# Kernel tuning notes

Hardware: AMD Instinct MI355X
Metric: run time of the kernel (lower is better)

## Reference

```python
import jax, jax.numpy as jnp
import numpy as np

N_NODES = 100000
N_EDGES = 1600000
N_FEAT = 64
DIM = 32
N_CLASSES = 10
N_GRAPHS = 64
BN_EPS = 1e-5


def setup_inputs() -> dict:
    key = jax.random.key(0)
    ks = jax.random.split(key, 20)
    x = jax.random.normal(ks[0], (N_NODES, N_FEAT), dtype=jnp.float32)
    edge_index = jax.random.randint(ks[1], (2, N_EDGES), 0, N_NODES, dtype=jnp.int64)
    batch = jnp.sort(jax.random.randint(ks[2], (N_NODES,), 0, N_GRAPHS, dtype=jnp.int64))
    s = 0.1
    # conv1 MLP (in=N_FEAT)
    w1a = jax.random.normal(ks[3], (N_FEAT, DIM), dtype=jnp.float32) * s
    b1a = jnp.zeros((DIM,), jnp.float32)
    w1b = jax.random.normal(ks[4], (DIM, DIM), dtype=jnp.float32) * s
    b1b = jnp.zeros((DIM,), jnp.float32)
    # convs 2-5 MLPs stacked [4, DIM, DIM]
    Wa = jax.random.normal(ks[5], (4, DIM, DIM), dtype=jnp.float32) * s
    Ba = jnp.zeros((4, DIM), jnp.float32)
    Wb = jax.random.normal(ks[6], (4, DIM, DIM), dtype=jnp.float32) * s
    Bb = jnp.zeros((4, DIM), jnp.float32)
    bn_gamma = jnp.ones((5, DIM), jnp.float32)
    bn_beta = jnp.zeros((5, DIM), jnp.float32)
    fc1_w = jax.random.normal(ks[7], (DIM, DIM), dtype=jnp.float32) * s
    fc1_b = jnp.zeros((DIM,), jnp.float32)
    fc2_w = jax.random.normal(ks[8], (DIM, N_CLASSES), dtype=jnp.float32) * s
    fc2_b = jnp.zeros((N_CLASSES,), jnp.float32)
    return dict(x=x, edge_index=edge_index, batch=batch,
                w1a=w1a, b1a=b1a, w1b=w1b, b1b=b1b,
                Wa=Wa, Ba=Ba, Wb=Wb, Bb=Bb,
                bn_gamma=bn_gamma, bn_beta=bn_beta,
                fc1_w=fc1_w, fc1_b=fc1_b, fc2_w=fc2_w, fc2_b=fc2_b)


def _gin_aggr(x, src, dst):
    # sum_{j in N(i)} x_j  + x_i   (eps = 0)
    agg = jax.ops.segment_sum(x[src], dst, num_segments=N_NODES)
    return x + agg


def _mlp(h, wa, ba, wb, bb):
    return jax.nn.relu(h @ wa + ba) @ wb + bb


def _bn(h, gamma, beta):
    mu = jnp.mean(h, axis=0)
    var = jnp.mean((h - mu) ** 2, axis=0)  # biased, torch BN training mode
    return (h - mu) * jax.lax.rsqrt(var + BN_EPS) * gamma + beta


def reference(x, edge_index, batch, w1a, b1a, w1b, b1b, Wa, Ba, Wb, Bb,
              bn_gamma, bn_beta, fc1_w, fc1_b, fc2_w, fc2_b):
    src, dst = edge_index[0], edge_index[1]
    # layer 1 (num_features -> dim)
    h = _mlp(_gin_aggr(x, src, dst), w1a, b1a, w1b, b1b)
    h = _bn(jax.nn.relu(h), bn_gamma[0], bn_beta[0])
    # layers 2-5 (dim -> dim)
    for i in range(4):
        h = _mlp(_gin_aggr(h, src, dst), Wa[i], Ba[i], Wb[i], Bb[i])
        h = _bn(jax.nn.relu(h), bn_gamma[i + 1], bn_beta[i + 1])
    # global add pool over graphs
    g = jax.ops.segment_sum(h, batch, num_segments=N_GRAPHS)  # [G, dim]
    g = jax.nn.relu(g @ fc1_w + fc1_b)
    # dropout: eval mode -> identity
    return g @ fc2_w + fc2_b  # [G, num_classes]
```

## Files before the change

kernel.cpp:

```cpp
#include <hip/hip_runtime.h>

#define NN 100000
#define NE 1600000
#define NF 64
#define DM 32
#define NG 64
#define NC 10
#define BN_EPS 1e-5f

#define BSHIFT 8
#define NBUCK ((NN + 255) >> 8)
#define CHUNK 8192
#define NCH ((NE + CHUNK - 1) / CHUNK)

__global__ __launch_bounds__(256) void binA_k(const int* __restrict__ ei,
                                              int* __restrict__ bcnt) {
    __shared__ int h[NBUCK];
    for (int i = threadIdx.x; i < NBUCK; i += 256) h[i] = 0;
    __syncthreads();
    long long base = (long long)blockIdx.x * CHUNK;
    int n = (int)((NE - base < CHUNK) ? (NE - base) : CHUNK);
    for (int i = threadIdx.x; i < n; i += 256) {
        int d = ei[NE + base + i];
        atomicAdd(&h[d >> BSHIFT], 1);
    }
    __syncthreads();
    for (int i = threadIdx.x; i < NBUCK; i += 256)
        if (h[i]) atomicAdd(&bcnt[i], h[i]);
}

__global__ __launch_bounds__(512) void binB_k(const int* __restrict__ bcnt,
                                              int* __restrict__ bbase,
                                              int* __restrict__ bcur) {
    __shared__ int s[512];
    int t = threadIdx.x;
    int v = (t < NBUCK) ? bcnt[t] : 0;
    s[t] = v;
    __syncthreads();
    int acc = v;
    for (int off = 1; off < 512; off <<= 1) {
        int add = (t >= off) ? s[t - off] : 0;
        __syncthreads();
        acc += add;
        s[t] = acc;
        __syncthreads();
    }
    if (t < NBUCK) { bbase[t] = acc - v; bcur[t] = acc - v; }
    if (t == 0) bbase[NBUCK] = NE;
}

__global__ __launch_bounds__(256) void binC_k(const int* __restrict__ ei,
                                              int* __restrict__ bcur,
                                              int2* __restrict__ binned) {
    __shared__ int cnt[NBUCK];
    __shared__ int ofs[NBUCK];
    __shared__ int idx[NBUCK];
    for (int i = threadIdx.x; i < NBUCK; i += 256) { cnt[i] = 0; idx[i] = 0; }
    __syncthreads();
    long long base = (long long)blockIdx.x * CHUNK;
    int n = (int)((NE - base < CHUNK) ? (NE - base) : CHUNK);
    int d[CHUNK / 256];
#pragma unroll
    for (int k = 0; k < CHUNK / 256; k++) {
        int i = threadIdx.x + k * 256;
        int dd = (i < n) ? ei[NE + base + i] : -1;
        d[k] = dd;
        if (dd >= 0) atomicAdd(&cnt[dd >> BSHIFT], 1);
    }
    __syncthreads();
    for (int i = threadIdx.x; i < NBUCK; i += 256)
        if (cnt[i]) ofs[i] = atomicAdd(&bcur[i], cnt[i]);
    __syncthreads();
#pragma unroll
    for (int k = 0; k < CHUNK / 256; k++) {
        int i = threadIdx.x + k * 256;
        if (i < n) {
            int src = ei[base + i];
            int b = d[k] >> BSHIFT;
            int l = atomicAdd(&idx[b], 1);
            binned[ofs[b] + l] = make_int2(src, d[k]);
        }
    }
}

__global__ __launch_bounds__(256) void binD_k(const int2* __restrict__ binned,
                                              const int* __restrict__ bbase,
                                              int* __restrict__ rowptr,
                                              int* __restrict__ csr) {
    __shared__ int cnt[256];
    __shared__ int cur[256];
    __shared__ int s[256];
    int b = blockIdx.x;
    int n0 = b << BSHIFT;
    int e0 = bbase[b], e1 = bbase[b + 1];
    int t = threadIdx.x;
    cnt[t] = 0;
    __syncthreads();
    for (int e = e0 + t; e < e1; e += 256) atomicAdd(&cnt[binned[e].y - n0], 1);
    __syncthreads();
    int v = cnt[t];
    s[t] = v;
    __syncthreads();
    int acc = v;
    for (int off = 1; off < 256; off <<= 1) {
        int add = (t >= off) ? s[t - off] : 0;
        __syncthreads();
        acc += add;
        s[t] = acc;
        __syncthreads();
    }
    int base = e0 + acc - v;
    int node = n0 + t;
    if (node < NN) rowptr[node] = base;
    cur[t] = base;
    if (b == NBUCK - 1 && t == 0) rowptr[NN] = NE;
    __syncthreads();
    for (int e = e0 + t; e < e1; e += 256) {
        int2 ed = binned[e];
        int p = atomicAdd(&cur[ed.y - n0], 1);
        csr[p] = ed.x;
    }
}

__global__ __launch_bounds__(256) void gather64_k(const float* __restrict__ x,
                                                  const int* __restrict__ rowptr,
                                                  const int* __restrict__ csr,
                                                  float* __restrict__ agg) {
    int tid = threadIdx.x;
    int node = blockIdx.x * 16 + tid / 16;
    int l = tid % 16;
    if (node >= NN) return;
    int s = rowptr[node], e = rowptr[node + 1];
    const float4* x4 = reinterpret_cast<const float4*>(x);
    float4 acc = make_float4(0.f, 0.f, 0.f, 0.f);
    for (int i = s; i < e; i++) {
        int src = csr[i];
        float4 v = x4[(long long)src * 16 + l];
        acc.x += v.x; acc.y += v.y; acc.z += v.z; acc.w += v.w;
    }
    reinterpret_cast<float4*>(agg)[(long long)node * 16 + l] = acc;
}

__global__ __launch_bounds__(256) void gather_bn_k(const float* __restrict__ h,
                                                   const int* __restrict__ rowptr,
                                                   const int* __restrict__ csr,
                                                   float* __restrict__ agg,
                                                   const float* __restrict__ st,
                                                   const float* __restrict__ gamma,
                                                   const float* __restrict__ beta) {
    int tid = threadIdx.x;
    int node = blockIdx.x * 32 + tid / 8;
    int l = tid % 8;
    if (node >= NN) return;
    const float invn = 1.0f / NN;
    float sc[4], sh[4];
#pragma unroll
    for (int c = 0; c < 4; c++) {
        int f = 4 * l + c;
        float mu = st[f] * invn;
        float var = st[32 + f] * invn - mu * mu;
        float scale = rsqrtf(var + BN_EPS) * gamma[f];
        sc[c] = scale;
        sh[c] = beta[f] - mu * scale;
    }
    int s = rowptr[node], e = rowptr[node + 1];
    const float4* h4 = reinterpret_cast<const float4*>(h);
    float4 acc = make_float4(0.f, 0.f, 0.f, 0.f);
    for (int i = s; i < e; i++) {
        int src = csr[i];
        float4 v = h4[(long long)src * 8 + l];
        acc.x += v.x; acc.y += v.y; acc.z += v.z; acc.w += v.w;
    }
    float deg = (float)(e - s);
    acc.x = acc.x * sc[0] + deg * sh[0];
    acc.y = acc.y * sc[1] + deg * sh[1];
    acc.z = acc.z * sc[2] + deg * sh[2];
    acc.w = acc.w * sc[3] + deg * sh[3];
    reinterpret_cast<float4*>(agg)[(long long)node * 8 + l] = acc;
}

__global__ __launch_bounds__(256) void mlp1_k(const float* __restrict__ x,
                                              const float* __restrict__ agg,
                                              const float* __restrict__ wa,
                                              const float* __restrict__ ba,
                                              const float* __restrict__ wb,
                                              const float* __restrict__ bb,
                                              float* __restrict__ out,
                                              float* __restrict__ stats) {
    __shared__ float sWa[64 * 32];
    __shared__ float sWb[32 * 32];
    __shared__ float sBa[32], sBb[32];
    __shared__ float sSum[4 * 32], sSq[4 * 32];
    int tid = threadIdx.x;
    for (int i = tid; i < 64 * 32; i += 256) sWa[i] = wa[i];
    for (int i = tid; i < 32 * 32; i += 256) sWb[i] = wb[i];
    if (tid < 32) { sBa[tid] = ba[tid]; sBb[tid] = bb[tid]; }
    __syncthreads();

    int node = blockIdx.x * 256 + tid;
    float r[32];
    if (node < NN) {
        float t[32];
#pragma unroll
        for (int j = 0; j < 32; j++) t[j] = sBa[j];
        const float4* xr = reinterpret_cast<const float4*>(x + (long long)node * 64);
        const float4* ar = reinterpret_cast<const float4*>(agg + (long long)node * 64);
        const float4* w4 = reinterpret_cast<const float4*>(sWa);
        for (int k4 = 0; k4 < 16; k4++) {
            float4 xv = xr[k4];
            float4 av = ar[k4];
            float a0 = xv.x + av.x, a1 = xv.y + av.y, a2 = xv.z + av.z, a3 = xv.w + av.w;
            int kb = k4 * 4;
#pragma unroll
            for (int q = 0; q < 8; q++) {
                float4 w0 = w4[(kb + 0) * 8 + q];
                float4 w1 = w4[(kb + 1) * 8 + q];
                float4 w2 = w4[(kb + 2) * 8 + q];
                float4 w3 = w4[(kb + 3) * 8 + q];
                t[4 * q + 0] += a0 * w0.x + a1 * w1.x + a2 * w2.x + a3 * w3.x;
                t[4 * q + 1] += a0 * w0.y + a1 * w1.y + a2 * w2.y + a3 * w3.y;
                t[4 * q + 2] += a0 * w0.z + a1 * w1.z + a2 * w2.z + a3 * w3.z;
                t[4 * q + 3] += a0 * w0.w + a1 * w1.w + a2 * w2.w + a3 * w3.w;
            }
        }
#pragma unroll
        for (int j = 0; j < 32; j++) t[j] = fmaxf(t[j], 0.f);
#pragma unroll
        for (int j = 0; j < 32; j++) r[j] = sBb[j];
        const float4* v4 = reinterpret_cast<const float4*>(sWb);
        for (int k = 0; k < 32; k++) {
            float a = t[k];
#pragma unroll
            for (int q = 0; q < 8; q++) {
                float4 w = v4[k * 8 + q];
                r[4 * q + 0] += a * w.x;
                r[4 * q + 1] += a * w.y;
                r[4 * q + 2] += a * w.z;
                r[4 * q + 3] += a * w.w;
            }
        }
#pragma unroll
        for (int j = 0; j < 32; j++) r[j] = fmaxf(r[j], 0.f);
        float4* orow = reinterpret_cast<float4*>(out + (long long)node * 32);
#pragma unroll
        for (int q = 0; q < 8; q++) {
            float4 o;
            o.x = r[4 * q]; o.y = r[4 * q + 1]; o.z = r[4 * q + 2]; o.w = r[4 * q + 3];
            orow[q] = o;
        }
    } else {
#pragma unroll
        for (int j = 0; j < 32; j++) r[j] = 0.f;
    }

    int lane = tid & 63, wid = tid >> 6;
#pragma unroll
    for (int j = 0; j < 32; j++) {
        float v = r[j], v2 = v * v;
#pragma unroll
        for (int off = 32; off >= 1; off >>= 1) {
            v += __shfl_down(v, off, 64);
            v2 += __shfl_down(v2, off, 64);
        }
        if (lane == 0) { sSum[wid * 32 + j] = v; sSq[wid * 32 + j] = v2; }
    }
    __syncthreads();
    if (tid < 32) {
        float a = sSum[tid] + sSum[32 + tid] + sSum[64 + tid] + sSum[96 + tid];
        float b = sSq[tid] + sSq[32 + tid] + sSq[64 + tid] + sSq[96 + tid];
        atomicAdd(&stats[tid], a);
        atomicAdd(&stats[32 + tid], b);
    }
}

__global__ __launch_bounds__(256) void mlp32_bn_k(float* __restrict__ h,
                                                  const float* __restrict__ agg,
                                                  const float* __restrict__ wa,
                                                  const float* __restrict__ ba,
                                                  const float* __restrict__ wb,
                                                  const float* __restrict__ bb,
                                                  const float* __restrict__ st,
                                                  const float* __restrict__ gamma,
                                                  const float* __restrict__ beta,
                                                  float* __restrict__ statsOut) {
    __shared__ float sWa[32 * 32];
    __shared__ float sWb[32 * 32];
    __shared__ float sBa[32], sBb[32];
    __shared__ float sSc[32], sSh[32];
    __shared__ float sSum[4 * 32], sSq[4 * 32];
    int tid = threadIdx.x;
    for (int i = tid; i < 32 * 32; i += 256) { sWa[i] = wa[i]; sWb[i] = wb[i]; }
    if (tid < 32) {
        sBa[tid] = ba[tid]; sBb[tid] = bb[tid];
        const float invn = 1.0f / NN;
        float mu = st[tid] * invn;
        float var = st[32 + tid] * invn - mu * mu;
        float scale = rsqrtf(var + BN_EPS) * gamma[tid];
        sSc[tid] = scale;
        sSh[tid] = beta[tid] - mu * scale;
    }
    __syncthreads();

    int node = blockIdx.x * 256 + tid;
    float r[32];
    if (node < NN) {
        float t[32];
#pragma unroll
        for (int j = 0; j < 32; j++) t[j] = sBa[j];
        const float4* hr = reinterpret_cast<const float4*>(h + (long long)node * 32);
        const float4* ar = reinterpret_cast<const float4*>(agg + (long long)node * 32);
        const float4* w4 = reinterpret_cast<const float4*>(sWa);
        for (int k4 = 0; k4 < 8; k4++) {
            float4 xv = hr[k4];
            float4 av = ar[k4];
            int kb = k4 * 4;
            float a0 = xv.x * sSc[kb + 0] + sSh[kb + 0] + av.x;
            float a1 = xv.y * sSc[kb + 1] + sSh[kb + 1] + av.y;
            float a2 = xv.z * sSc[kb + 2] + sSh[kb + 2] + av.z;
            float a3 = xv.w * sSc[kb + 3] + sSh[kb + 3] + av.w;
#pragma unroll
            for (int q = 0; q < 8; q++) {
                float4 w0 = w4[(kb + 0) * 8 + q];
                float4 w1 = w4[(kb + 1) * 8 + q];
                float4 w2 = w4[(kb + 2) * 8 + q];
                float4 w3 = w4[(kb + 3) * 8 + q];
                t[4 * q + 0] += a0 * w0.x + a1 * w1.x + a2 * w2.x + a3 * w3.x;
                t[4 * q + 1] += a0 * w0.y + a1 * w1.y + a2 * w2.y + a3 * w3.y;
                t[4 * q + 2] += a0 * w0.z + a1 * w1.z + a2 * w2.z + a3 * w3.z;
                t[4 * q + 3] += a0 * w0.w + a1 * w1.w + a2 * w2.w + a3 * w3.w;
            }
        }
#pragma unroll
        for (int j = 0; j < 32; j++) t[j] = fmaxf(t[j], 0.f);
#pragma unroll
        for (int j = 0; j < 32; j++) r[j] = sBb[j];
        const float4* v4 = reinterpret_cast<const float4*>(sWb);
        for (int k = 0; k < 32; k++) {
            float a = t[k];
#pragma unroll
            for (int q = 0; q < 8; q++) {
                float4 w = v4[k * 8 + q];
                r[4 * q + 0] += a * w.x;
                r[4 * q + 1] += a * w.y;
                r[4 * q + 2] += a * w.z;
                r[4 * q + 3] += a * w.w;
            }
        }
#pragma unroll
        for (int j = 0; j < 32; j++) r[j] = fmaxf(r[j], 0.f);
        float4* orow = reinterpret_cast<float4*>(h + (long long)node * 32);
#pragma unroll
        for (int q = 0; q < 8; q++) {
            float4 o;
            o.x = r[4 * q]; o.y = r[4 * q + 1]; o.z = r[4 * q + 2]; o.w = r[4 * q + 3];
            orow[q] = o;
        }
    } else {
#pragma unroll
        for (int j = 0; j < 32; j++) r[j] = 0.f;
    }

    int lane = tid & 63, wid = tid >> 6;
#pragma unroll
    for (int j = 0; j < 32; j++) {
        float v = r[j], v2 = v * v;
#pragma unroll
        for (int off = 32; off >= 1; off >>= 1) {
            v += __shfl_down(v, off, 64);
            v2 += __shfl_down(v2, off, 64);
        }
        if (lane == 0) { sSum[wid * 32 + j] = v; sSq[wid * 32 + j] = v2; }
    }
    __syncthreads();
    if (tid < 32) {
        float a = sSum[tid] + sSum[32 + tid] + sSum[64 + tid] + sSum[96 + tid];
        float b = sSq[tid] + sSq[32 + tid] + sSq[64 + tid] + sSq[96 + tid];
        atomicAdd(&statsOut[tid], a);
        atomicAdd(&statsOut[32 + tid], b);
    }
}

#define POOL_NPB 512
__global__ __launch_bounds__(256) void pool_bn_k(const float* __restrict__ h,
                                                 const int* __restrict__ batch,
                                                 const float* __restrict__ st,
                                                 const float* __restrict__ gamma,
                                                 const float* __restrict__ beta,
                                                 float* __restrict__ pooled) {
    int tid = threadIdx.x;
    int f = tid & 31;
    int p = tid >> 5;
    int n0 = blockIdx.x * POOL_NPB + p * (POOL_NPB / 8);
    int n1 = n0 + POOL_NPB / 8;
    if (n1 > NN) n1 = NN;
    if (n0 >= NN) return;
    const float invn = 1.0f / NN;
    float mu = st[f] * invn;
    float var = st[32 + f] * invn - mu * mu;
    float sc = rsqrtf(var + BN_EPS) * gamma[f];
    float sh = beta[f] - mu * sc;
    float acc = 0.f;
    int cur = batch[n0];
    for (int n = n0; n < n1; n++) {
        int g = batch[n];
        if (g != cur) {
            atomicAdd(&pooled[cur * 32 + f], acc);
            cur = g;
            acc = 0.f;
        }
        acc += h[(long long)n * 32 + f] * sc + sh;
    }
    atomicAdd(&pooled[cur * 32 + f], acc);
}

__global__ __launch_bounds__(64) void final_k(const float* __restrict__ pooled,
                                              const float* __restrict__ w1,
                                              const float* __restrict__ b1,
                                              const float* __restrict__ w2,
                                              const float* __restrict__ b2,
                                              float* __restrict__ out) {
    int g = threadIdx.x;
    if (g >= NG) return;
    float t[32];
#pragma unroll
    for (int j = 0; j < 32; j++) t[j] = b1[j];
    for (int k = 0; k < 32; k++) {
        float a = pooled[g * 32 + k];
#pragma unroll
        for (int j = 0; j < 32; j++) t[j] += a * w1[k * 32 + j];
    }
#pragma unroll
    for (int j = 0; j < 32; j++) t[j] = fmaxf(t[j], 0.f);
    for (int c = 0; c < NC; c++) {
        float o = b2[c];
#pragma unroll
        for (int k = 0; k < 32; k++) o += t[k] * w2[k * NC + c];
        out[g * NC + c] = o;
    }
}

extern "C" void kernel_launch(void* const* d_in, const int* in_sizes, int n_in,
                              void* d_out, int out_size, void* d_ws, size_t ws_size,
                              hipStream_t stream) {
    const float* x = (const float*)d_in[0];
    const int* ei = (const int*)d_in[1];
    const int* batch = (const int*)d_in[2];
    const float* w1a = (const float*)d_in[3];
    const float* b1a = (const float*)d_in[4];
    const float* w1b = (const float*)d_in[5];
    const float* b1b = (const float*)d_in[6];
    const float* Wa = (const float*)d_in[7];
    const float* Ba = (const float*)d_in[8];
    const float* Wb = (const float*)d_in[9];
    const float* Bb = (const float*)d_in[10];
    const float* bn_gamma = (const float*)d_in[11];
    const float* bn_beta = (const float*)d_in[12];
    const float* fc1w = (const float*)d_in[13];
    const float* fc1b = (const float*)d_in[14];
    const float* fc2w = (const float*)d_in[15];
    const float* fc2b = (const float*)d_in[16];
    float* out = (float*)d_out;

    float* ws = (float*)d_ws;
    float* agg = ws;
    float* hb = agg + (size_t)NN * 64;
    float* stats_all = hb + (size_t)NN * 32;
    float* pooled = stats_all + 5 * 64;
    int2* binned = (int2*)(pooled + NG * 32);
    int* bcnt = (int*)(binned + NE);
    int* bbase = bcnt + NBUCK;
    int* bcur = bbase + NBUCK + 1;
    int* rowptr = bcur + NBUCK;
    int* csr = rowptr + NN + 1;

    const int nodeBlocks = (NN + 255) / 256;

    hipMemsetAsync(bcnt, 0, NBUCK * sizeof(int), stream);
    binA_k<<<NCH, 256, 0, stream>>>(ei, bcnt);
    binB_k<<<1, 512, 0, stream>>>(bcnt, bbase, bcur);
    binC_k<<<NCH, 256, 0, stream>>>(ei, bcur, binned);
    binD_k<<<NBUCK, 256, 0, stream>>>(binned, bbase, rowptr, csr);

    hipMemsetAsync(stats_all, 0, 5 * 64 * sizeof(float), stream);
    hipMemsetAsync(pooled, 0, NG * 32 * sizeof(float), stream);

    gather64_k<<<NN / 16, 256, 0, stream>>>(x, rowptr, csr, agg);
    mlp1_k<<<nodeBlocks, 256, 0, stream>>>(x, agg, w1a, b1a, w1b, b1b, hb, stats_all);

    for (int i = 0; i < 4; i++) {
        const float* st = stats_all + i * 64;
        const float* g = bn_gamma + i * 32;
        const float* be = bn_beta + i * 32;
        gather_bn_k<<<NN / 32, 256, 0, stream>>>(hb, rowptr, csr, agg, st, g, be);
        mlp32_bn_k<<<nodeBlocks, 256, 0, stream>>>(hb, agg, Wa + i * 1024, Ba + i * 32,
                                                   Wb + i * 1024, Bb + i * 32,
                                                   st, g, be, stats_all + (i + 1) * 64);
    }

    pool_bn_k<<<(NN + POOL_NPB - 1) / POOL_NPB, 256, 0, stream>>>(
        hb, batch, stats_all + 4 * 64, bn_gamma + 4 * 32, bn_beta + 4 * 32, pooled);
    final_k<<<1, 64, 0, stream>>>(pooled, fc1w, fc1b, fc2w, fc2b, out);
}
```

Baseline: 589.4 us.

## Project layer-1 features before aggregation, pack binned edges, unroll gathers

Layer 1 now multiplies x by W1a before the neighbour aggregation (linearity), so the gather reads 32-float rows instead of 64-float rows. This halves the random-access traffic of the first gather, at the cost of an extra projection kernel and an intermediate buffer. Binned edges are packed into one 32-bit word (src<<8 | local dst), which halves binning traffic but limits src to 24 bits. Gather loops are unrolled by two with separate accumulators to keep more loads in flight, and the two memsets are merged into one.

```diff
diff --git a/kernel.cpp b/kernel.cpp
--- a/kernel.cpp
+++ b/kernel.cpp
@@ -51,7 +51,7 @@
 
 __global__ __launch_bounds__(256) void binC_k(const int* __restrict__ ei,
                                               int* __restrict__ bcur,
-                                              int2* __restrict__ binned) {
+                                              unsigned* __restrict__ binned) {
     __shared__ int cnt[NBUCK];
     __shared__ int ofs[NBUCK];
     __shared__ int idx[NBUCK];
@@ -75,15 +75,15 @@
     for (int k = 0; k < CHUNK / 256; k++) {
         int i = threadIdx.x + k * 256;
         if (i < n) {
-            int src = ei[base + i];
+            unsigned src = (unsigned)ei[base + i];
             int b = d[k] >> BSHIFT;
             int l = atomicAdd(&idx[b], 1);
-            binned[ofs[b] + l] = make_int2(src, d[k]);
-        }
-    }
-}
-
-__global__ __launch_bounds__(256) void binD_k(const int2* __restrict__ binned,
+            binned[ofs[b] + l] = (src << 8) | (unsigned)(d[k] & 255);
+        }
+    }
+}
+
+__global__ __launch_bounds__(256) void binD_k(const unsigned* __restrict__ binned,
                                               const int* __restrict__ bbase,
                                               int* __restrict__ rowptr,
                                               int* __restrict__ csr) {
@@ -91,12 +91,11 @@
     __shared__ int cur[256];
     __shared__ int s[256];
     int b = blockIdx.x;
-    int n0 = b << BSHIFT;
     int e0 = bbase[b], e1 = bbase[b + 1];
     int t = threadIdx.x;
     cnt[t] = 0;
     __syncthreads();
-    for (int e = e0 + t; e < e1; e += 256) atomicAdd(&cnt[binned[e].y - n0], 1);
+    for (int e = e0 + t; e < e1; e += 256) atomicAdd(&cnt[binned[e] & 255u], 1);
     __syncthreads();
     int v = cnt[t];
     s[t] = v;
@@ -110,35 +109,82 @@
         __syncthreads();
     }
     int base = e0 + acc - v;
-    int node = n0 + t;
+    int node = (b << BSHIFT) + t;
     if (node < NN) rowptr[node] = base;
     cur[t] = base;
     if (b == NBUCK - 1 && t == 0) rowptr[NN] = NE;
     __syncthreads();
     for (int e = e0 + t; e < e1; e += 256) {
-        int2 ed = binned[e];
-        int p = atomicAdd(&cur[ed.y - n0], 1);
-        csr[p] = ed.x;
-    }
-}
-
-__global__ __launch_bounds__(256) void gather64_k(const float* __restrict__ x,
+        unsigned w = binned[e];
+        int p = atomicAdd(&cur[w & 255u], 1);
+        csr[p] = (int)(w >> 8);
+    }
+}
+
+__global__ __launch_bounds__(256) void pre1_k(const float* __restrict__ x,
+                                              const float* __restrict__ wa,
+                                              float* __restrict__ y) {
+    __shared__ float sWa[64 * 32];
+    int tid = threadIdx.x;
+    for (int i = tid; i < 64 * 32; i += 256) sWa[i] = wa[i];
+    __syncthreads();
+    int node = blockIdx.x * 256 + tid;
+    if (node >= NN) return;
+    float t[32];
+#pragma unroll
+    for (int j = 0; j < 32; j++) t[j] = 0.f;
+    const float4* xr = reinterpret_cast<const float4*>(x + (long long)node * 64);
+    const float4* w4 = reinterpret_cast<const float4*>(sWa);
+    for (int k4 = 0; k4 < 16; k4++) {
+        float4 xv = xr[k4];
+        int kb = k4 * 4;
+#pragma unroll
+        for (int q = 0; q < 8; q++) {
+            float4 w0 = w4[(kb + 0) * 8 + q];
+            float4 w1 = w4[(kb + 1) * 8 + q];
+            float4 w2 = w4[(kb + 2) * 8 + q];
+            float4 w3 = w4[(kb + 3) * 8 + q];
+            t[4 * q + 0] += xv.x * w0.x + xv.y * w1.x + xv.z * w2.x + xv.w * w3.x;
+            t[4 * q + 1] += xv.x * w0.y + xv.y * w1.y + xv.z * w2.y + xv.w * w3.y;
+            t[4 * q + 2] += xv.x * w0.z + xv.y * w1.z + xv.z * w2.z + xv.w * w3.z;
+            t[4 * q + 3] += xv.x * w0.w + xv.y * w1.w + xv.z * w2.w + xv.w * w3.w;
+        }
+    }
+    float4* yr = reinterpret_cast<float4*>(y + (long long)node * 32);
+#pragma unroll
+    for (int q = 0; q < 8; q++) {
+        float4 o;
+        o.x = t[4 * q]; o.y = t[4 * q + 1]; o.z = t[4 * q + 2]; o.w = t[4 * q + 3];
+        yr[q] = o;
+    }
+}
+
+__global__ __launch_bounds__(256) void gather32_k(const float* __restrict__ y,
                                                   const int* __restrict__ rowptr,
                                                   const int* __restrict__ csr,
                                                   float* __restrict__ agg) {
     int tid = threadIdx.x;
-    int node = blockIdx.x * 16 + tid / 16;
-    int l = tid % 16;
+    int node = blockIdx.x * 32 + tid / 8;
+    int l = tid % 8;
     if (node >= NN) return;
     int s = rowptr[node], e = rowptr[node + 1];
-    const float4* x4 = reinterpret_cast<const float4*>(x);
-    float4 acc = make_float4(0.f, 0.f, 0.f, 0.f);
-    for (int i = s; i < e; i++) {
-        int src = csr[i];
-        float4 v = x4[(long long)src * 16 + l];
-        acc.x += v.x; acc.y += v.y; acc.z += v.z; acc.w += v.w;
-    }
-    reinterpret_cast<float4*>(agg)[(long long)node * 16 + l] = acc;
+    const float4* y4 = reinterpret_cast<const float4*>(y);
+    float4 a0 = make_float4(0.f, 0.f, 0.f, 0.f);
+    float4 a1 = make_float4(0.f, 0.f, 0.f, 0.f);
+    int i = s;
+    for (; i + 2 <= e; i += 2) {
+        int s0 = csr[i], s1 = csr[i + 1];
+        float4 v0 = y4[(long long)s0 * 8 + l];
+        float4 v1 = y4[(long long)s1 * 8 + l];
+        a0.x += v0.x; a0.y += v0.y; a0.z += v0.z; a0.w += v0.w;
+        a1.x += v1.x; a1.y += v1.y; a1.z += v1.z; a1.w += v1.w;
+    }
+    if (i < e) {
+        float4 v = y4[(long long)csr[i] * 8 + l];
+        a0.x += v.x; a0.y += v.y; a0.z += v.z; a0.w += v.w;
+    }
+    a0.x += a1.x; a0.y += a1.y; a0.z += a1.z; a0.w += a1.w;
+    reinterpret_cast<float4*>(agg)[(long long)node * 8 + l] = a0;
 }
 
 __global__ __launch_bounds__(256) void gather_bn_k(const float* __restrict__ h,
@@ -165,34 +211,40 @@
     }
     int s = rowptr[node], e = rowptr[node + 1];
     const float4* h4 = reinterpret_cast<const float4*>(h);
-    float4 acc = make_float4(0.f, 0.f, 0.f, 0.f);
-    for (int i = s; i < e; i++) {
-        int src = csr[i];
-        float4 v = h4[(long long)src * 8 + l];
-        acc.x += v.x; acc.y += v.y; acc.z += v.z; acc.w += v.w;
-    }
+    float4 a0 = make_float4(0.f, 0.f, 0.f, 0.f);
+    float4 a1 = make_float4(0.f, 0.f, 0.f, 0.f);
+    int i = s;
+    for (; i + 2 <= e; i += 2) {
+        int s0 = csr[i], s1 = csr[i + 1];
+        float4 v0 = h4[(long long)s0 * 8 + l];
+        float4 v1 = h4[(long long)s1 * 8 + l];
+        a0.x += v0.x; a0.y += v0.y; a0.z += v0.z; a0.w += v0.w;
+        a1.x += v1.x; a1.y += v1.y; a1.z += v1.z; a1.w += v1.w;
+    }
+    if (i < e) {
+        float4 v = h4[(long long)csr[i] * 8 + l];
+        a0.x += v.x; a0.y += v.y; a0.z += v.z; a0.w += v.w;
+    }
+    a0.x += a1.x; a0.y += a1.y; a0.z += a1.z; a0.w += a1.w;
     float deg = (float)(e - s);
-    acc.x = acc.x * sc[0] + deg * sh[0];
-    acc.y = acc.y * sc[1] + deg * sh[1];
-    acc.z = acc.z * sc[2] + deg * sh[2];
-    acc.w = acc.w * sc[3] + deg * sh[3];
-    reinterpret_cast<float4*>(agg)[(long long)node * 8 + l] = acc;
-}
-
-__global__ __launch_bounds__(256) void mlp1_k(const float* __restrict__ x,
-                                              const float* __restrict__ agg,
-                                              const float* __restrict__ wa,
-                                              const float* __restrict__ ba,
-                                              const float* __restrict__ wb,
-                                              const float* __restrict__ bb,
-                                              float* __restrict__ out,
-                                              float* __restrict__ stats) {
-    __shared__ float sWa[64 * 32];
+    a0.x = a0.x * sc[0] + deg * sh[0];
+    a0.y = a0.y * sc[1] + deg * sh[1];
+    a0.z = a0.z * sc[2] + deg * sh[2];
+    a0.w = a0.w * sc[3] + deg * sh[3];
+    reinterpret_cast<float4*>(agg)[(long long)node * 8 + l] = a0;
+}
+
+__global__ __launch_bounds__(256) void mlp1b_k(const float* __restrict__ y,
+                                               const float* __restrict__ agg,
+                                               const float* __restrict__ ba,
+                                               const float* __restrict__ wb,
+                                               const float* __restrict__ bb,
+                                               float* __restrict__ out,
+                                               float* __restrict__ stats) {
     __shared__ float sWb[32 * 32];
     __shared__ float sBa[32], sBb[32];
     __shared__ float sSum[4 * 32], sSq[4 * 32];
     int tid = threadIdx.x;
-    for (int i = tid; i < 64 * 32; i += 256) sWa[i] = wa[i];
     for (int i = tid; i < 32 * 32; i += 256) sWb[i] = wb[i];
     if (tid < 32) { sBa[tid] = ba[tid]; sBb[tid] = bb[tid]; }
     __syncthreads();
@@ -200,43 +252,29 @@
     int node = blockIdx.x * 256 + tid;
     float r[32];
     if (node < NN) {
-        float t[32];
-#pragma unroll
-        for (int j = 0; j < 32; j++) t[j] = sBa[j];
-        const float4* xr = reinterpret_cast<const float4*>(x + (long long)node * 64);
-        const float4* ar = reinterpret_cast<const float4*>(agg + (long long)node * 64);
-        const float4* w4 = reinterpret_cast<const float4*>(sWa);
-        for (int k4 = 0; k4 < 16; k4++) {
-            float4 xv = xr[k4];
-            float4 av = ar[k4];
-            float a0 = xv.x + av.x, a1 = xv.y + av.y, a2 = xv.z + av.z, a3 = xv.w + av.w;
-            int kb = k4 * 4;
-#pragma unroll
-            for (int q = 0; q < 8; q++) {
-                float4 w0 = w4[(kb + 0) * 8 + q];
-                float4 w1 = w4[(kb + 1) * 8 + q];
-                float4 w2 = w4[(kb + 2) * 8 + q];
-                float4 w3 = w4[(kb + 3) * 8 + q];
-                t[4 * q + 0] += a0 * w0.x + a1 * w1.x + a2 * w2.x + a3 * w3.x;
-                t[4 * q + 1] += a0 * w0.y + a1 * w1.y + a2 * w2.y + a3 * w3.y;
-                t[4 * q + 2] += a0 * w0.z + a1 * w1.z + a2 * w2.z + a3 * w3.z;
-                t[4 * q + 3] += a0 * w0.w + a1 * w1.w + a2 * w2.w + a3 * w3.w;
-            }
-        }
-#pragma unroll
-        for (int j = 0; j < 32; j++) t[j] = fmaxf(t[j], 0.f);
+        const float4* yr = reinterpret_cast<const float4*>(y + (long long)node * 32);
+        const float4* ar = reinterpret_cast<const float4*>(agg + (long long)node * 32);
 #pragma unroll
         for (int j = 0; j < 32; j++) r[j] = sBb[j];
         const float4* v4 = reinterpret_cast<const float4*>(sWb);
-        for (int k = 0; k < 32; k++) {
-            float a = t[k];
+        for (int k4 = 0; k4 < 8; k4++) {
+            float4 yv = yr[k4];
+            float4 av = ar[k4];
+            int kb = k4 * 4;
+            float t0 = fmaxf(yv.x + av.x + sBa[kb + 0], 0.f);
+            float t1 = fmaxf(yv.y + av.y + sBa[kb + 1], 0.f);
+            float t2 = fmaxf(yv.z + av.z + sBa[kb + 2], 0.f);
+            float t3 = fmaxf(yv.w + av.w + sBa[kb + 3], 0.f);
 #pragma unroll
             for (int q = 0; q < 8; q++) {
-                float4 w = v4[k * 8 + q];
-                r[4 * q + 0] += a * w.x;
-                r[4 * q + 1] += a * w.y;
-                r[4 * q + 2] += a * w.z;
-                r[4 * q + 3] += a * w.w;
+                float4 w0 = v4[(kb + 0) * 8 + q];
+                float4 w1 = v4[(kb + 1) * 8 + q];
+                float4 w2 = v4[(kb + 2) * 8 + q];
+                float4 w3 = v4[(kb + 3) * 8 + q];
+                r[4 * q + 0] += t0 * w0.x + t1 * w1.x + t2 * w2.x + t3 * w3.x;
+                r[4 * q + 1] += t0 * w0.y + t1 * w1.y + t2 * w2.y + t3 * w3.y;
+                r[4 * q + 2] += t0 * w0.z + t1 * w1.z + t2 * w2.z + t3 * w3.z;
+                r[4 * q + 3] += t0 * w0.w + t1 * w1.w + t2 * w2.w + t3 * w3.w;
             }
         }
 #pragma unroll
@@ -462,11 +500,12 @@
     float* out = (float*)d_out;
 
     float* ws = (float*)d_ws;
-    float* agg = ws;
-    float* hb = agg + (size_t)NN * 64;
-    float* stats_all = hb + (size_t)NN * 32;
+    float* y = ws;
+    float* hb = y + (size_t)NN * 32;
+    float* agg = hb + (size_t)NN * 32;
+    float* stats_all = agg + (size_t)NN * 32;
     float* pooled = stats_all + 5 * 64;
-    int2* binned = (int2*)(pooled + NG * 32);
+    unsigned* binned = (unsigned*)(pooled + NG * 32);
     int* bcnt = (int*)(binned + NE);
     int* bbase = bcnt + NBUCK;
     int* bcur = bbase + NBUCK + 1;
@@ -474,6 +513,7 @@
     int* csr = rowptr + NN + 1;
 
     const int nodeBlocks = (NN + 255) / 256;
+    const int gBlocks = (NN + 31) / 32;
 
     hipMemsetAsync(bcnt, 0, NBUCK * sizeof(int), stream);
     binA_k<<<NCH, 256, 0, stream>>>(ei, bcnt);
@@ -481,17 +521,17 @@
     binC_k<<<NCH, 256, 0, stream>>>(ei, bcur, binned);
     binD_k<<<NBUCK, 256, 0, stream>>>(binned, bbase, rowptr, csr);
 
-    hipMemsetAsync(stats_all, 0, 5 * 64 * sizeof(float), stream);
-    hipMemsetAsync(pooled, 0, NG * 32 * sizeof(float), stream);
-
-    gather64_k<<<NN / 16, 256, 0, stream>>>(x, rowptr, csr, agg);
-    mlp1_k<<<nodeBlocks, 256, 0, stream>>>(x, agg, w1a, b1a, w1b, b1b, hb, stats_all);
+    hipMemsetAsync(stats_all, 0, (5 * 64 + NG * 32) * sizeof(float), stream);
+
+    pre1_k<<<nodeBlocks, 256, 0, stream>>>(x, w1a, y);
+    gather32_k<<<gBlocks, 256, 0, stream>>>(y, rowptr, csr, agg);
+    mlp1b_k<<<nodeBlocks, 256, 0, stream>>>(y, agg, b1a, w1b, b1b, hb, stats_all);
 
     for (int i = 0; i < 4; i++) {
         const float* st = stats_all + i * 64;
         const float* g = bn_gamma + i * 32;
         const float* be = bn_beta + i * 32;
-        gather_bn_k<<<NN / 32, 256, 0, stream>>>(hb, rowptr, csr, agg, st, g, be);
+        gather_bn_k<<<gBlocks, 256, 0, stream>>>(hb, rowptr, csr, agg, st, g, be);
         mlp32_bn_k<<<nodeBlocks, 256, 0, stream>>>(hb, agg, Wa + i * 1024, Ba + i * 32,
                                                    Wb + i * 1024, Bb + i * 32,
                                                    st, g, be, stats_all + (i + 1) * 64);
```

After: 525.3 us. 10.9% less time.
